# Kernel tuning notes

Hardware: AMD Instinct MI355X
Metric: run time of the kernel (lower is better)

## Reference

```python
import jax, jax.numpy as jnp
import numpy as np

B, T, F, H, S = 4096, 256, 64, 128, 32


def setup_inputs() -> dict:
    key = jax.random.key(0)
    ks = jax.random.split(key, 10)
    return {
        "x": jax.random.normal(ks[0], (B, T, F), jnp.float32),
        "static": jax.random.normal(ks[1], (B, S), jnp.float32),
        "hs0": jax.random.normal(ks[2], (B, H), jnp.float32),
        "cs0": jax.random.normal(ks[3], (B, H), jnp.float32),
        "W_ih": jax.random.normal(ks[4], (4 * H, F), jnp.float32) * 0.1,
        "W_hh": jax.random.normal(ks[5], (4 * H, H), jnp.float32) * 0.1,
        "b_ih": jax.random.normal(ks[6], (4 * H,), jnp.float32) * 0.1,
        "b_hh": jax.random.normal(ks[7], (4 * H,), jnp.float32) * 0.1,
        "W_lin": jax.random.normal(ks[8], (1, H + S), jnp.float32) * 0.1,
        "b_lin": jax.random.normal(ks[9], (1,), jnp.float32) * 0.1,
    }


def reference(x, static, hs0, cs0, W_ih, W_hh, b_ih, b_hh, W_lin, b_lin):
    # x: [B, T, F] -> time-major [T, B, F]; precompute input projections for all steps
    xs = jnp.swapaxes(x, 0, 1)
    px = jnp.einsum('tbf,gf->tbg', xs, W_ih) + b_ih  # [T, B, 4H]

    def step(carry, px_t):
        h, c = carry
        gates = px_t + h @ W_hh.T + b_hh  # [B, 4H]
        i, f, g, o = jnp.split(gates, 4, axis=-1)  # PyTorch LSTM gate order
        i = jax.nn.sigmoid(i)
        f = jax.nn.sigmoid(f)
        g = jnp.tanh(g)
        o = jax.nn.sigmoid(o)
        c = f * c + i * g
        h = o * jnp.tanh(c)
        return (h, c), None

    (h, c), _ = jax.lax.scan(step, (hs0, cs0), px)
    full = jnp.concatenate([h, static], axis=1)  # [B, H+S]
    return full @ W_lin.T + b_lin  # [B, 1]
```

## Files before the change

kernel.cpp:

```cpp
#include <hip/hip_runtime.h>
#include <hip/hip_bf16.h>

#define B_ 4096
#define T_ 256
#define F_ 64
#define H_ 128
#define S_ 32

typedef __attribute__((ext_vector_type(8))) short bf16x8;
typedef __attribute__((ext_vector_type(4))) float f32x4;

#define XS 72
#define HS 136

#define K1f (-1.4426950408889634f)
#define K2f (-2.8853900817779268f)

__device__ __forceinline__ float bf2f(unsigned short u) {
    unsigned v = (unsigned)u << 16;
    return __builtin_bit_cast(float, v);
}
__device__ __forceinline__ short f2bs(float f) {
    return (short)__bfloat16_as_ushort(__float2bfloat16(f));
}

#define LSTM_PHASE(XR, HR, HW, XW, STAGE_EN)                                      \
  {                                                                               \
    float2 xpre;                                                                  \
    const bool st_ = (STAGE_EN);                                                  \
    if (st_) xpre = *(const float2*)gxp;                                          \
    bf16x8 a[6];                                                                  \
    a[0] = *(const bf16x8*)&XR[fxb];                                              \
    a[1] = *(const bf16x8*)&XR[fxb + 32];                                         \
    a[2] = *(const bf16x8*)&HR[fhb];                                              \
    a[3] = *(const bf16x8*)&HR[fhb + 32];                                         \
    a[4] = *(const bf16x8*)&HR[fhb + 64];                                         \
    a[5] = *(const bf16x8*)&HR[fhb + 96];                                         \
    f32x4 ac[4];                                                                  \
    _Pragma("unroll")                                                             \
    for (int g = 0; g < 4; ++g)                                                   \
      ac[g] = __builtin_amdgcn_mfma_f32_16x16x32_bf16(wf[g][0], a[0], z4, 0, 0, 0); \
    _Pragma("unroll")                                                             \
    for (int kt = 1; kt < 6; ++kt) {                                              \
      _Pragma("unroll")                                                           \
      for (int g = 0; g < 4; ++g)                                                 \
        ac[g] = __builtin_amdgcn_mfma_f32_16x16x32_bf16(wf[g][kt], a[kt], ac[g], 0, 0, 0); \
    }                                                                             \
    float hn[4];                                                                  \
    _Pragma("unroll")                                                             \
    for (int q = 0; q < 4; ++q) {                                                 \
      const float ei = __builtin_amdgcn_exp2f(__builtin_fmaf(ac[0][q], K1f, bs0[q])); \
      const float i_ = __builtin_amdgcn_rcpf(1.0f + ei);                          \
      const float ef = __builtin_amdgcn_exp2f(__builtin_fmaf(ac[1][q], K1f, bs1[q])); \
      const float f_ = __builtin_amdgcn_rcpf(1.0f + ef);                          \
      const float eg = __builtin_amdgcn_exp2f(__builtin_fmaf(ac[2][q], K2f, btn[q])); \
      const float g_ = __builtin_fmaf(2.0f, __builtin_amdgcn_rcpf(1.0f + eg), -1.0f); \
      const float eo = __builtin_amdgcn_exp2f(__builtin_fmaf(ac[3][q], K1f, bs3[q])); \
      const float o_ = __builtin_amdgcn_rcpf(1.0f + eo);                          \
      const float cn = __builtin_fmaf(f_, c[q], i_ * g_);                         \
      c[q] = cn;                                                                  \
      const float ec = __builtin_amdgcn_exp2f(cn * K2f);                          \
      const float th = __builtin_fmaf(2.0f, __builtin_amdgcn_rcpf(1.0f + ec), -1.0f); \
      hn[q] = o_ * th;                                                            \
    }                                                                             \
    {                                                                             \
      float2 p0; p0.x = hn[0]; p0.y = hn[1];                                      \
      float2 p1; p1.x = hn[2]; p1.y = hn[3];                                      \
      __hip_bfloat162 b01 = __float22bfloat162_rn(p0);                            \
      __hip_bfloat162 b23 = __float22bfloat162_rn(p1);                            \
      uint2 uv; uv.x = *(unsigned*)&b01; uv.y = *(unsigned*)&b23;                 \
      *(uint2*)&HW[hwo] = uv;                                                     \
    }                                                                             \
    if (st_) {                                                                    \
      __hip_bfloat162 qx = __float22bfloat162_rn(xpre);                           \
      *(__hip_bfloat162*)&XW[xwo] = qx;                                           \
      gxp += F_;                                                                  \
    }                                                                             \
    __syncthreads();                                                              \
  }

__global__ __launch_bounds__(512, 2) void lstm_fused_kernel(
    const float* __restrict__ x,
    const float* __restrict__ statik,
    const float* __restrict__ hs0,
    const float* __restrict__ cs0,
    const float* __restrict__ W_ih,
    const float* __restrict__ W_hh,
    const float* __restrict__ b_ih,
    const float* __restrict__ b_hh,
    const float* __restrict__ W_lin,
    const float* __restrict__ b_lin,
    float* __restrict__ out)
{
    __shared__ unsigned short x_l[2][16 * XS];
    __shared__ unsigned short h_l[2][16 * HS];

    const int tid  = threadIdx.x;
    const int lane = tid & 63;
    const int w    = tid >> 6;
    const int b0   = blockIdx.x * 16;

    const int lrow = lane & 15;
    const int lkb  = lane >> 4;
    const int n0q  = w * 16 + lkb * 4;

    bf16x8 wf[4][6];
    #pragma unroll
    for (int g = 0; g < 4; ++g) {
        const int n = g * 128 + w * 16 + lrow;
        #pragma unroll
        for (int kt = 0; kt < 6; ++kt) {
            const int k0 = kt * 32 + lkb * 8;
            const float* src = (kt < 2) ? (W_ih + n * F_ + k0)
                                        : (W_hh + n * H_ + (k0 - 64));
            const float4 s0 = *(const float4*)(src);
            const float4 s1 = *(const float4*)(src + 4);
            bf16x8 v;
            v[0] = f2bs(s0.x); v[1] = f2bs(s0.y); v[2] = f2bs(s0.z); v[3] = f2bs(s0.w);
            v[4] = f2bs(s1.x); v[5] = f2bs(s1.y); v[6] = f2bs(s1.z); v[7] = f2bs(s1.w);
            wf[g][kt] = v;
        }
    }

    float bs0[4], bs1[4], btn[4], bs3[4];
    #pragma unroll
    for (int g = 0; g < 4; ++g) {
        const float4 bi = *(const float4*)(b_ih + g * 128 + n0q);
        const float4 bh = *(const float4*)(b_hh + g * 128 + n0q);
        const float bq[4] = {bi.x + bh.x, bi.y + bh.y, bi.z + bh.z, bi.w + bh.w};
        #pragma unroll
        for (int q = 0; q < 4; ++q) {
            if (g == 0)      bs0[q] = bq[q] * K1f;
            else if (g == 1) bs1[q] = bq[q] * K1f;
            else if (g == 2) btn[q] = bq[q] * K2f;
            else             bs3[q] = bq[q] * K1f;
        }
    }

    float c[4];
    {
        const float4 cv = *(const float4*)(cs0 + (size_t)(b0 + lrow) * H_ + n0q);
        c[0] = cv.x; c[1] = cv.y; c[2] = cv.z; c[3] = cv.w;
    }

    const int srow = tid >> 5;
    const int scp  = tid & 31;
    {
        const float* hp = hs0 + (size_t)(b0 + srow) * H_ + scp * 2;
        const float2 hv0 = *(const float2*)(hp);
        const float2 hv1 = *(const float2*)(hp + 64);
        __hip_bfloat162 q0 = __float22bfloat162_rn(hv0);
        __hip_bfloat162 q1 = __float22bfloat162_rn(hv1);
        *(__hip_bfloat162*)&h_l[0][srow * HS + scp * 2]      = q0;
        *(__hip_bfloat162*)&h_l[0][srow * HS + 64 + scp * 2] = q1;
    }
    const float* gxp = x + (size_t)(b0 + srow) * (T_ * F_) + scp * 2;
    {
        const float2 xv = *(const float2*)gxp;
        __hip_bfloat162 qx = __float22bfloat162_rn(xv);
        *(__hip_bfloat162*)&x_l[0][srow * XS + scp * 2] = qx;
    }
    gxp += F_;
    __syncthreads();

    const int fxb = lrow * XS + lkb * 8;
    const int fhb = lrow * HS + lkb * 8;
    const int hwo = lrow * HS + n0q;
    const int xwo = srow * XS + scp * 2;
    const f32x4 z4 = {0.0f, 0.0f, 0.0f, 0.0f};

    for (int t = 0; t < T_; t += 2) {
        LSTM_PHASE(x_l[0], h_l[0], h_l[1], x_l[1], true);
        LSTM_PHASE(x_l[1], h_l[1], h_l[0], x_l[0], (t + 2 < T_));
    }

    {
        const unsigned short* hf = h_l[0];
        const float wl0 = W_lin[lane];
        const float wl1 = W_lin[64 + lane];
        const float wl2 = (lane < S_) ? W_lin[128 + lane] : 0.0f;
        const float bl  = b_lin[0];
        #pragma unroll
        for (int rr = 0; rr < 2; ++rr) {
            const int r = w * 2 + rr;
            float p = bf2f(hf[r * HS + lane]) * wl0
                    + bf2f(hf[r * HS + 64 + lane]) * wl1;
            if (lane < S_) p += statik[(size_t)(b0 + r) * S_ + lane] * wl2;
            #pragma unroll
            for (int m = 32; m > 0; m >>= 1) p += __shfl_xor(p, m, 64);
            if (lane == 0) out[b0 + r] = p + bl;
        }
    }
}

extern "C" void kernel_launch(void* const* d_in, const int* in_sizes, int n_in,
                              void* d_out, int out_size, void* d_ws, size_t ws_size,
                              hipStream_t stream) {
    const float* x     = (const float*)d_in[0];
    const float* st    = (const float*)d_in[1];
    const float* hs0   = (const float*)d_in[2];
    const float* cs0   = (const float*)d_in[3];
    const float* W_ih  = (const float*)d_in[4];
    const float* W_hh  = (const float*)d_in[5];
    const float* b_ih  = (const float*)d_in[6];
    const float* b_hh  = (const float*)d_in[7];
    const float* W_lin = (const float*)d_in[8];
    const float* b_lin = (const float*)d_in[9];
    float* out = (float*)d_out;

    lstm_fused_kernel<<<dim3(B_ / 16), dim3(512), 0, stream>>>(
        x, st, hs0, cs0, W_ih, W_hh, b_ih, b_hh, W_lin, b_lin, out);
}
```

Baseline: 254.7 us.

## Load x directly into per-lane MFMA fragments, drop LDS staging of x

Each lane now loads its own x fragment for the input-projection MFMAs straight from global memory into registers, prefetching two steps ahead, and converts it to bf16 in registers. This removes the x shared-memory buffer, the staging stores and the LDS reads of x on every step. The barrier is replaced by an explicit lgkmcnt wait plus s_barrier, so it no longer waits on outstanding global loads. The cost is more VGPRs for the two in-flight x register sets and redundant global loads, since each x row is now read by several waves instead of once per block.

Result: slower. 316.0 us (+24.1%).

```diff
diff --git a/kernel.cpp b/kernel.cpp
--- a/kernel.cpp
+++ b/kernel.cpp
@@ -10,7 +10,6 @@
 typedef __attribute__((ext_vector_type(8))) short bf16x8;
 typedef __attribute__((ext_vector_type(4))) float f32x4;
 
-#define XS 72
 #define HS 136
 
 #define K1f (-1.4426950408889634f)
@@ -24,38 +23,67 @@
     return (short)__bfloat16_as_ushort(__float2bfloat16(f));
 }
 
-#define LSTM_PHASE(XR, HR, HW, XW, STAGE_EN)                                      \
+struct XReg { float4 a, b, c, d; };
+
+#define PHASE(XR, HR, HW, TL)                                                     \
   {                                                                               \
-    float2 xpre;                                                                  \
-    const bool st_ = (STAGE_EN);                                                  \
-    if (st_) xpre = *(const float2*)gxp;                                          \
-    bf16x8 a[6];                                                                  \
-    a[0] = *(const bf16x8*)&XR[fxb];                                              \
-    a[1] = *(const bf16x8*)&XR[fxb + 32];                                         \
-    a[2] = *(const bf16x8*)&HR[fhb];                                              \
-    a[3] = *(const bf16x8*)&HR[fhb + 32];                                         \
-    a[4] = *(const bf16x8*)&HR[fhb + 64];                                         \
-    a[5] = *(const bf16x8*)&HR[fhb + 96];                                         \
-    f32x4 ac[4];                                                                  \
-    _Pragma("unroll")                                                             \
-    for (int g = 0; g < 4; ++g)                                                   \
-      ac[g] = __builtin_amdgcn_mfma_f32_16x16x32_bf16(wf[g][0], a[0], z4, 0, 0, 0); \
-    _Pragma("unroll")                                                             \
-    for (int kt = 1; kt < 6; ++kt) {                                              \
-      _Pragma("unroll")                                                           \
-      for (int g = 0; g < 4; ++g)                                                 \
-        ac[g] = __builtin_amdgcn_mfma_f32_16x16x32_bf16(wf[g][kt], a[kt], ac[g], 0, 0, 0); \
-    }                                                                             \
+                        \
+    bf16x8 a0 = *(const bf16x8*)&HR[fhb];                                         \
+    bf16x8 a1 = *(const bf16x8*)&HR[fhb + 32];                                    \
+    bf16x8 a2 = *(const bf16x8*)&HR[fhb + 64];                                    \
+    bf16x8 a3 = *(const bf16x8*)&HR[fhb + 96];                                    \
+          \
+    bf16x8 fx0, fx1;                                                              \
+    fx0[0] = f2bs(XR.a.x); fx0[1] = f2bs(XR.a.y); fx0[2] = f2bs(XR.a.z);          \
+    fx0[3] = f2bs(XR.a.w); fx0[4] = f2bs(XR.b.x); fx0[5] = f2bs(XR.b.y);          \
+    fx0[6] = f2bs(XR.b.z); fx0[7] = f2bs(XR.b.w);                                 \
+    fx1[0] = f2bs(XR.c.x); fx1[1] = f2bs(XR.c.y); fx1[2] = f2bs(XR.c.z);          \
+    fx1[3] = f2bs(XR.c.w); fx1[4] = f2bs(XR.d.x); fx1[5] = f2bs(XR.d.y);          \
+    fx1[6] = f2bs(XR.d.z); fx1[7] = f2bs(XR.d.w);                                 \
+         \
+    { const float* lp_ = gxl + (size_t)(TL) * F_;                                 \
+      XR.a = *(const float4*)(lp_);                                               \
+      XR.b = *(const float4*)(lp_ + 4);                                           \
+      XR.c = *(const float4*)(lp_ + 32);                                          \
+      XR.d = *(const float4*)(lp_ + 36); }                                        \
+            \
+    f32x4 ac0, ac1, ac2, ac3;                                                     \
+    ac0 = __builtin_amdgcn_mfma_f32_16x16x32_bf16(wf[0][0], fx0, z4, 0, 0, 0);    \
+    ac1 = __builtin_amdgcn_mfma_f32_16x16x32_bf16(wf[1][0], fx0, z4, 0, 0, 0);    \
+    ac2 = __builtin_amdgcn_mfma_f32_16x16x32_bf16(wf[2][0], fx0, z4, 0, 0, 0);    \
+    ac3 = __builtin_amdgcn_mfma_f32_16x16x32_bf16(wf[3][0], fx0, z4, 0, 0, 0);    \
+    ac0 = __builtin_amdgcn_mfma_f32_16x16x32_bf16(wf[0][1], fx1, ac0, 0, 0, 0);   \
+    ac1 = __builtin_amdgcn_mfma_f32_16x16x32_bf16(wf[1][1], fx1, ac1, 0, 0, 0);   \
+    ac2 = __builtin_amdgcn_mfma_f32_16x16x32_bf16(wf[2][1], fx1, ac2, 0, 0, 0);   \
+    ac3 = __builtin_amdgcn_mfma_f32_16x16x32_bf16(wf[3][1], fx1, ac3, 0, 0, 0);   \
+                                                                      \
+    ac0 = __builtin_amdgcn_mfma_f32_16x16x32_bf16(wf[0][2], a0, ac0, 0, 0, 0);    \
+    ac1 = __builtin_amdgcn_mfma_f32_16x16x32_bf16(wf[1][2], a0, ac1, 0, 0, 0);    \
+    ac2 = __builtin_amdgcn_mfma_f32_16x16x32_bf16(wf[2][2], a0, ac2, 0, 0, 0);    \
+    ac3 = __builtin_amdgcn_mfma_f32_16x16x32_bf16(wf[3][2], a0, ac3, 0, 0, 0);    \
+    ac0 = __builtin_amdgcn_mfma_f32_16x16x32_bf16(wf[0][3], a1, ac0, 0, 0, 0);    \
+    ac1 = __builtin_amdgcn_mfma_f32_16x16x32_bf16(wf[1][3], a1, ac1, 0, 0, 0);    \
+    ac2 = __builtin_amdgcn_mfma_f32_16x16x32_bf16(wf[2][3], a1, ac2, 0, 0, 0);    \
+    ac3 = __builtin_amdgcn_mfma_f32_16x16x32_bf16(wf[3][3], a1, ac3, 0, 0, 0);    \
+    ac0 = __builtin_amdgcn_mfma_f32_16x16x32_bf16(wf[0][4], a2, ac0, 0, 0, 0);    \
+    ac1 = __builtin_amdgcn_mfma_f32_16x16x32_bf16(wf[1][4], a2, ac1, 0, 0, 0);    \
+    ac2 = __builtin_amdgcn_mfma_f32_16x16x32_bf16(wf[2][4], a2, ac2, 0, 0, 0);    \
+    ac3 = __builtin_amdgcn_mfma_f32_16x16x32_bf16(wf[3][4], a2, ac3, 0, 0, 0);    \
+    ac0 = __builtin_amdgcn_mfma_f32_16x16x32_bf16(wf[0][5], a3, ac0, 0, 0, 0);    \
+    ac1 = __builtin_amdgcn_mfma_f32_16x16x32_bf16(wf[1][5], a3, ac1, 0, 0, 0);    \
+    ac2 = __builtin_amdgcn_mfma_f32_16x16x32_bf16(wf[2][5], a3, ac2, 0, 0, 0);    \
+    ac3 = __builtin_amdgcn_mfma_f32_16x16x32_bf16(wf[3][5], a3, ac3, 0, 0, 0);    \
+                                                  \
     float hn[4];                                                                  \
     _Pragma("unroll")                                                             \
     for (int q = 0; q < 4; ++q) {                                                 \
-      const float ei = __builtin_amdgcn_exp2f(__builtin_fmaf(ac[0][q], K1f, bs0[q])); \
+      const float ei = __builtin_amdgcn_exp2f(__builtin_fmaf(ac0[q], K1f, bs0[q])); \
       const float i_ = __builtin_amdgcn_rcpf(1.0f + ei);                          \
-      const float ef = __builtin_amdgcn_exp2f(__builtin_fmaf(ac[1][q], K1f, bs1[q])); \
+      const float ef = __builtin_amdgcn_exp2f(__builtin_fmaf(ac1[q], K1f, bs1[q])); \
       const float f_ = __builtin_amdgcn_rcpf(1.0f + ef);                          \
-      const float eg = __builtin_amdgcn_exp2f(__builtin_fmaf(ac[2][q], K2f, btn[q])); \
+      const float eg = __builtin_amdgcn_exp2f(__builtin_fmaf(ac2[q], K2f, btn[q])); \
       const float g_ = __builtin_fmaf(2.0f, __builtin_amdgcn_rcpf(1.0f + eg), -1.0f); \
-      const float eo = __builtin_amdgcn_exp2f(__builtin_fmaf(ac[3][q], K1f, bs3[q])); \
+      const float eo = __builtin_amdgcn_exp2f(__builtin_fmaf(ac3[q], K1f, bs3[q])); \
       const float o_ = __builtin_amdgcn_rcpf(1.0f + eo);                          \
       const float cn = __builtin_fmaf(f_, c[q], i_ * g_);                         \
       c[q] = cn;                                                                  \
@@ -63,20 +91,14 @@
       const float th = __builtin_fmaf(2.0f, __builtin_amdgcn_rcpf(1.0f + ec), -1.0f); \
       hn[q] = o_ * th;                                                            \
     }                                                                             \
-    {                                                                             \
-      float2 p0; p0.x = hn[0]; p0.y = hn[1];                                      \
-      float2 p1; p1.x = hn[2]; p1.y = hn[3];                                      \
-      __hip_bfloat162 b01 = __float22bfloat162_rn(p0);                            \
-      __hip_bfloat162 b23 = __float22bfloat162_rn(p1);                            \
-      uint2 uv; uv.x = *(unsigned*)&b01; uv.y = *(unsigned*)&b23;                 \
-      *(uint2*)&HW[hwo] = uv;                                                     \
-    }                                                                             \
-    if (st_) {                                                                    \
-      __hip_bfloat162 qx = __float22bfloat162_rn(xpre);                           \
-      *(__hip_bfloat162*)&XW[xwo] = qx;                                           \
-      gxp += F_;                                                                  \
-    }                                                                             \
-    __syncthreads();                                                              \
+    { unsigned lo = (unsigned)(unsigned short)f2bs(hn[0])                         \
+                  | ((unsigned)(unsigned short)f2bs(hn[1]) << 16);                \
+      unsigned hi = (unsigned)(unsigned short)f2bs(hn[2])                         \
+                  | ((unsigned)(unsigned short)f2bs(hn[3]) << 16);                \
+      uint2 uv; uv.x = lo; uv.y = hi;                                             \
+      *(uint2*)&HW[hwo] = uv; }                                                   \
+    asm volatile("s_waitcnt lgkmcnt(0)" ::: "memory");                            \
+    __builtin_amdgcn_s_barrier();                                                 \
   }
 
 __global__ __launch_bounds__(512, 2) void lstm_fused_kernel(
@@ -92,7 +114,6 @@
     const float* __restrict__ b_lin,
     float* __restrict__ out)
 {
-    __shared__ unsigned short x_l[2][16 * XS];
     __shared__ unsigned short h_l[2][16 * HS];
 
     const int tid  = threadIdx.x;
@@ -143,35 +164,41 @@
         c[0] = cv.x; c[1] = cv.y; c[2] = cv.z; c[3] = cv.w;
     }
 
-    const int srow = tid >> 5;
-    const int scp  = tid & 31;
+    const float* gxl = x + (size_t)(b0 + lrow) * (T_ * F_) + lkb * 8;
+
     {
+        const int srow = tid >> 5;
+        const int scp  = tid & 31;
         const float* hp = hs0 + (size_t)(b0 + srow) * H_ + scp * 2;
         const float2 hv0 = *(const float2*)(hp);
         const float2 hv1 = *(const float2*)(hp + 64);
-        __hip_bfloat162 q0 = __float22bfloat162_rn(hv0);
-        __hip_bfloat162 q1 = __float22bfloat162_rn(hv1);
-        *(__hip_bfloat162*)&h_l[0][srow * HS + scp * 2]      = q0;
-        *(__hip_bfloat162*)&h_l[0][srow * HS + 64 + scp * 2] = q1;
-    }
-    const float* gxp = x + (size_t)(b0 + srow) * (T_ * F_) + scp * 2;
-    {
-        const float2 xv = *(const float2*)gxp;
-        __hip_bfloat162 qx = __float22bfloat162_rn(xv);
-        *(__hip_bfloat162*)&x_l[0][srow * XS + scp * 2] = qx;
-    }
-    gxp += F_;
+        unsigned q0 = (unsigned)(unsigned short)f2bs(hv0.x)
+                    | ((unsigned)(unsigned short)f2bs(hv0.y) << 16);
+        unsigned q1 = (unsigned)(unsigned short)f2bs(hv1.x)
+                    | ((unsigned)(unsigned short)f2bs(hv1.y) << 16);
+        *(unsigned*)&h_l[0][srow * HS + scp * 2]      = q0;
+        *(unsigned*)&h_l[0][srow * HS + 64 + scp * 2] = q1;
+    }
+    XReg xr0, xr1;
+    xr0.a = *(const float4*)(gxl);
+    xr0.b = *(const float4*)(gxl + 4);
+    xr0.c = *(const float4*)(gxl + 32);
+    xr0.d = *(const float4*)(gxl + 36);
+    xr1.a = *(const float4*)(gxl + F_);
+    xr1.b = *(const float4*)(gxl + F_ + 4);
+    xr1.c = *(const float4*)(gxl + F_ + 32);
+    xr1.d = *(const float4*)(gxl + F_ + 36);
     __syncthreads();
 
-    const int fxb = lrow * XS + lkb * 8;
     const int fhb = lrow * HS + lkb * 8;
     const int hwo = lrow * HS + n0q;
-    const int xwo = srow * XS + scp * 2;
     const f32x4 z4 = {0.0f, 0.0f, 0.0f, 0.0f};
 
     for (int t = 0; t < T_; t += 2) {
-        LSTM_PHASE(x_l[0], h_l[0], h_l[1], x_l[1], true);
-        LSTM_PHASE(x_l[1], h_l[1], h_l[0], x_l[0], (t + 2 < T_));
+        const int tl0 = (t + 2 < T_) ? t + 2 : T_ - 1;
+        const int tl1 = (t + 3 < T_) ? t + 3 : T_ - 1;
+        PHASE(xr0, h_l[0], h_l[1], tl0);
+        PHASE(xr1, h_l[1], h_l[0], tl1);
     }
 
     {
```

## Precompute next step's input-projection MFMAs off the critical path and swizzle LDS

Applied to the files above, without the earlier changes.

Splits the per-step MFMA chain so the x·W_ih part for the next timestep is issued after the gate math and carried in registers, leaving only the 4 h-dependent k-tiles on the recurrent critical path. The x staging becomes a 4-deep ring with a register-held prefetch several steps ahead. Padded LDS rows are replaced by XOR-swizzled layouts to avoid bank conflicts. The __syncthreads is replaced by an explicit lgkmcnt wait plus s_barrier. This adds register pressure and makes the buffer-index logic more delicate.

New measurement: 228.6 us. 10.2% less time.

```diff
diff --git a/kernel.cpp b/kernel.cpp
--- a/kernel.cpp
+++ b/kernel.cpp
@@ -10,11 +10,10 @@
 typedef __attribute__((ext_vector_type(8))) short bf16x8;
 typedef __attribute__((ext_vector_type(4))) float f32x4;
 
-#define XS 72
-#define HS 136
-
 #define K1f (-1.4426950408889634f)
 #define K2f (-2.8853900817779268f)
+
+#define MF(A, B, C) __builtin_amdgcn_mfma_f32_16x16x32_bf16((A), (B), (C), 0, 0, 0)
 
 __device__ __forceinline__ float bf2f(unsigned short u) {
     unsigned v = (unsigned)u << 16;
@@ -24,59 +23,61 @@
     return (short)__bfloat16_as_ushort(__float2bfloat16(f));
 }
 
-#define LSTM_PHASE(XR, HR, HW, XW, STAGE_EN)                                      \
-  {                                                                               \
-    float2 xpre;                                                                  \
-    const bool st_ = (STAGE_EN);                                                  \
-    if (st_) xpre = *(const float2*)gxp;                                          \
-    bf16x8 a[6];                                                                  \
-    a[0] = *(const bf16x8*)&XR[fxb];                                              \
-    a[1] = *(const bf16x8*)&XR[fxb + 32];                                         \
-    a[2] = *(const bf16x8*)&HR[fhb];                                              \
-    a[3] = *(const bf16x8*)&HR[fhb + 32];                                         \
-    a[4] = *(const bf16x8*)&HR[fhb + 64];                                         \
-    a[5] = *(const bf16x8*)&HR[fhb + 96];                                         \
-    f32x4 ac[4];                                                                  \
-    _Pragma("unroll")                                                             \
-    for (int g = 0; g < 4; ++g)                                                   \
-      ac[g] = __builtin_amdgcn_mfma_f32_16x16x32_bf16(wf[g][0], a[0], z4, 0, 0, 0); \
-    _Pragma("unroll")                                                             \
-    for (int kt = 1; kt < 6; ++kt) {                                              \
-      _Pragma("unroll")                                                           \
-      for (int g = 0; g < 4; ++g)                                                 \
-        ac[g] = __builtin_amdgcn_mfma_f32_16x16x32_bf16(wf[g][kt], a[kt], ac[g], 0, 0, 0); \
-    }                                                                             \
-    float hn[4];                                                                  \
-    _Pragma("unroll")                                                             \
-    for (int q = 0; q < 4; ++q) {                                                 \
-      const float ei = __builtin_amdgcn_exp2f(__builtin_fmaf(ac[0][q], K1f, bs0[q])); \
-      const float i_ = __builtin_amdgcn_rcpf(1.0f + ei);                          \
-      const float ef = __builtin_amdgcn_exp2f(__builtin_fmaf(ac[1][q], K1f, bs1[q])); \
-      const float f_ = __builtin_amdgcn_rcpf(1.0f + ef);                          \
-      const float eg = __builtin_amdgcn_exp2f(__builtin_fmaf(ac[2][q], K2f, btn[q])); \
+#define PHASE(HR, HW, XW, XN, TLD)                                               \
+  {                                                                              \
+    const char* hr_ = (const char*)(HR);                                         \
+    bf16x8 a0 = *(const bf16x8*)(hr_ + fh0);                                     \
+    bf16x8 a1 = *(const bf16x8*)(hr_ + fh1);                                     \
+    bf16x8 a2 = *(const bf16x8*)(hr_ + fh2);                                     \
+    bf16x8 a3 = *(const bf16x8*)(hr_ + fh3);                                     \
+                    \
+    { __hip_bfloat162 qx = __float22bfloat162_rn(xheld);                         \
+      *(__hip_bfloat162*)((char*)(XW) + xws) = qx; }                             \
+    xheld = *(const float2*)(gxs + (size_t)(TLD) * F_);                          \
+                                          \
+    f32x4 ac0 = sd0, ac1 = sd1, ac2 = sd2, ac3 = sd3;                            \
+    ac0 = MF(wf[0][2], a0, ac0); ac1 = MF(wf[1][2], a0, ac1);                    \
+    ac2 = MF(wf[2][2], a0, ac2); ac3 = MF(wf[3][2], a0, ac3);                    \
+    ac0 = MF(wf[0][3], a1, ac0); ac1 = MF(wf[1][3], a1, ac1);                    \
+    ac2 = MF(wf[2][3], a1, ac2); ac3 = MF(wf[3][3], a1, ac3);                    \
+    ac0 = MF(wf[0][4], a2, ac0); ac1 = MF(wf[1][4], a2, ac1);                    \
+    ac2 = MF(wf[2][4], a2, ac2); ac3 = MF(wf[3][4], a2, ac3);                    \
+    ac0 = MF(wf[0][5], a3, ac0); ac1 = MF(wf[1][5], a3, ac1);                    \
+    ac2 = MF(wf[2][5], a3, ac2); ac3 = MF(wf[3][5], a3, ac3);                    \
+                                                 \
+    float hn[4];                                                                 \
+    _Pragma("unroll")                                                            \
+    for (int q = 0; q < 4; ++q) {                                                \
+      const float ei = __builtin_amdgcn_exp2f(__builtin_fmaf(ac0[q], K1f, bs0[q])); \
+      const float i_ = __builtin_amdgcn_rcpf(1.0f + ei);                         \
+      const float ef = __builtin_amdgcn_exp2f(__builtin_fmaf(ac1[q], K1f, bs1[q])); \
+      const float f_ = __builtin_amdgcn_rcpf(1.0f + ef);                         \
+      const float eg = __builtin_amdgcn_exp2f(__builtin_fmaf(ac2[q], K2f, btn[q])); \
       const float g_ = __builtin_fmaf(2.0f, __builtin_amdgcn_rcpf(1.0f + eg), -1.0f); \
-      const float eo = __builtin_amdgcn_exp2f(__builtin_fmaf(ac[3][q], K1f, bs3[q])); \
-      const float o_ = __builtin_amdgcn_rcpf(1.0f + eo);                          \
-      const float cn = __builtin_fmaf(f_, c[q], i_ * g_);                         \
-      c[q] = cn;                                                                  \
-      const float ec = __builtin_amdgcn_exp2f(cn * K2f);                          \
+      const float eo = __builtin_amdgcn_exp2f(__builtin_fmaf(ac3[q], K1f, bs3[q])); \
+      const float o_ = __builtin_amdgcn_rcpf(1.0f + eo);                         \
+      const float cn = __builtin_fmaf(f_, c[q], i_ * g_);                        \
+      c[q] = cn;                                                                 \
+      const float ec = __builtin_amdgcn_exp2f(cn * K2f);                         \
       const float th = __builtin_fmaf(2.0f, __builtin_amdgcn_rcpf(1.0f + ec), -1.0f); \
-      hn[q] = o_ * th;                                                            \
-    }                                                                             \
-    {                                                                             \
-      float2 p0; p0.x = hn[0]; p0.y = hn[1];                                      \
-      float2 p1; p1.x = hn[2]; p1.y = hn[3];                                      \
-      __hip_bfloat162 b01 = __float22bfloat162_rn(p0);                            \
-      __hip_bfloat162 b23 = __float22bfloat162_rn(p1);                            \
-      uint2 uv; uv.x = *(unsigned*)&b01; uv.y = *(unsigned*)&b23;                 \
-      *(uint2*)&HW[hwo] = uv;                                                     \
-    }                                                                             \
-    if (st_) {                                                                    \
-      __hip_bfloat162 qx = __float22bfloat162_rn(xpre);                           \
-      *(__hip_bfloat162*)&XW[xwo] = qx;                                           \
-      gxp += F_;                                                                  \
-    }                                                                             \
-    __syncthreads();                                                              \
+      hn[q] = o_ * th;                                                           \
+    }                                                                            \
+    { float2 p0; p0.x = hn[0]; p0.y = hn[1];                                     \
+      float2 p1; p1.x = hn[2]; p1.y = hn[3];                                     \
+      __hip_bfloat162 b01 = __float22bfloat162_rn(p0);                           \
+      __hip_bfloat162 b23 = __float22bfloat162_rn(p1);                           \
+      uint2 uv; uv.x = *(unsigned*)&b01; uv.y = *(unsigned*)&b23;                \
+      *(uint2*)((char*)(HW) + hwb) = uv; }                                       \
+              \
+    { const char* xn_ = (const char*)(XN);                                       \
+      bf16x8 nf0 = *(const bf16x8*)(xn_ + fx0);                                  \
+      bf16x8 nf1 = *(const bf16x8*)(xn_ + fx1);                                  \
+      sd0 = MF(wf[0][0], nf0, z4); sd1 = MF(wf[1][0], nf0, z4);                  \
+      sd2 = MF(wf[2][0], nf0, z4); sd3 = MF(wf[3][0], nf0, z4);                  \
+      sd0 = MF(wf[0][1], nf1, sd0); sd1 = MF(wf[1][1], nf1, sd1);                \
+      sd2 = MF(wf[2][1], nf1, sd2); sd3 = MF(wf[3][1], nf1, sd3); }              \
+    asm volatile("s_waitcnt lgkmcnt(0)" ::: "memory");                           \
+    __builtin_amdgcn_s_barrier();                                                \
   }
 
 __global__ __launch_bounds__(512, 2) void lstm_fused_kernel(
@@ -92,8 +93,8 @@
     const float* __restrict__ b_lin,
     float* __restrict__ out)
 {
-    __shared__ unsigned short x_l[2][16 * XS];
-    __shared__ unsigned short h_l[2][16 * HS];
+    __shared__ __align__(16) unsigned short h_l[2][16 * 128];
+    __shared__ __align__(16) unsigned short x_l[4][16 * 64];
 
     const int tid  = threadIdx.x;
     const int lane = tid & 63;
@@ -143,48 +144,80 @@
         c[0] = cv.x; c[1] = cv.y; c[2] = cv.z; c[3] = cv.w;
     }
 
+    const int fsw = (lrow & 7) << 4;
+    const int fx0 = lrow * 128 + ((lkb * 16) ^ fsw);
+    const int fx1 = lrow * 128 + ((64 + lkb * 16) ^ fsw);
+    const int fh0 = lrow * 256 + ((0   + lkb * 16) ^ fsw);
+    const int fh1 = lrow * 256 + ((64  + lkb * 16) ^ fsw);
+    const int fh2 = lrow * 256 + ((128 + lkb * 16) ^ fsw);
+    const int fh3 = lrow * 256 + ((192 + lkb * 16) ^ fsw);
+    const int hwb = lrow * 256 + ((n0q * 2) ^ fsw);
+
     const int srow = tid >> 5;
     const int scp  = tid & 31;
+    const int ssw  = (srow & 7) << 4;
+    const int xws  = srow * 128 + ((scp * 4) ^ ssw);
+
+    const float* gxs = x + (size_t)(b0 + srow) * (T_ * F_) + scp * 2;
+    float2 xheld;
     {
         const float* hp = hs0 + (size_t)(b0 + srow) * H_ + scp * 2;
         const float2 hv0 = *(const float2*)(hp);
         const float2 hv1 = *(const float2*)(hp + 64);
         __hip_bfloat162 q0 = __float22bfloat162_rn(hv0);
         __hip_bfloat162 q1 = __float22bfloat162_rn(hv1);
-        *(__hip_bfloat162*)&h_l[0][srow * HS + scp * 2]      = q0;
-        *(__hip_bfloat162*)&h_l[0][srow * HS + 64 + scp * 2] = q1;
-    }
-    const float* gxp = x + (size_t)(b0 + srow) * (T_ * F_) + scp * 2;
-    {
-        const float2 xv = *(const float2*)gxp;
-        __hip_bfloat162 qx = __float22bfloat162_rn(xv);
-        *(__hip_bfloat162*)&x_l[0][srow * XS + scp * 2] = qx;
-    }
-    gxp += F_;
+        *(__hip_bfloat162*)((char*)h_l[0] + srow * 256 + ((scp * 4) ^ ssw))       = q0;
+        *(__hip_bfloat162*)((char*)h_l[0] + srow * 256 + ((128 + scp * 4) ^ ssw)) = q1;
+
+        const float2 x0 = *(const float2*)(gxs);
+        const float2 x1 = *(const float2*)(gxs + F_);
+        __hip_bfloat162 qa = __float22bfloat162_rn(x0);
+        __hip_bfloat162 qb = __float22bfloat162_rn(x1);
+        *(__hip_bfloat162*)((char*)x_l[0] + xws) = qa;
+        *(__hip_bfloat162*)((char*)x_l[1] + xws) = qb;
+        xheld = *(const float2*)(gxs + 2 * F_);
+    }
     __syncthreads();
 
-    const int fxb = lrow * XS + lkb * 8;
-    const int fhb = lrow * HS + lkb * 8;
-    const int hwo = lrow * HS + n0q;
-    const int xwo = srow * XS + scp * 2;
     const f32x4 z4 = {0.0f, 0.0f, 0.0f, 0.0f};
 
-    for (int t = 0; t < T_; t += 2) {
-        LSTM_PHASE(x_l[0], h_l[0], h_l[1], x_l[1], true);
-        LSTM_PHASE(x_l[1], h_l[1], h_l[0], x_l[0], (t + 2 < T_));
-    }
-
-    {
-        const unsigned short* hf = h_l[0];
+    f32x4 sd0, sd1, sd2, sd3;
+    {
+        const char* xn_ = (const char*)x_l[0];
+        bf16x8 nf0 = *(const bf16x8*)(xn_ + fx0);
+        bf16x8 nf1 = *(const bf16x8*)(xn_ + fx1);
+        sd0 = MF(wf[0][0], nf0, z4); sd1 = MF(wf[1][0], nf0, z4);
+        sd2 = MF(wf[2][0], nf0, z4); sd3 = MF(wf[3][0], nf0, z4);
+        sd0 = MF(wf[0][1], nf1, sd0); sd1 = MF(wf[1][1], nf1, sd1);
+        sd2 = MF(wf[2][1], nf1, sd2); sd3 = MF(wf[3][1], nf1, sd3);
+    }
+
+    for (int t = 0; t < T_; t += 4) {
+        const int t3 = (t + 3 < T_) ? t + 3 : T_ - 1;
+        const int t4 = (t + 4 < T_) ? t + 4 : T_ - 1;
+        const int t5 = (t + 5 < T_) ? t + 5 : T_ - 1;
+        const int t6 = (t + 6 < T_) ? t + 6 : T_ - 1;
+        PHASE(h_l[0], h_l[1], x_l[2], x_l[1], t3);
+        PHASE(h_l[1], h_l[0], x_l[3], x_l[2], t4);
+        PHASE(h_l[0], h_l[1], x_l[0], x_l[3], t5);
+        PHASE(h_l[1], h_l[0], x_l[1], x_l[0], t6);
+    }
+
+    {
+        const char* hf = (const char*)h_l[0];
         const float wl0 = W_lin[lane];
         const float wl1 = W_lin[64 + lane];
         const float wl2 = (lane < S_) ? W_lin[128 + lane] : 0.0f;
         const float bl  = b_lin[0];
         #pragma unroll
         for (int rr = 0; rr < 2; ++rr) {
-            const int r = w * 2 + rr;
-            float p = bf2f(hf[r * HS + lane]) * wl0
-                    + bf2f(hf[r * HS + 64 + lane]) * wl1;
+            const int r  = w * 2 + rr;
+            const int rs = (r & 7) << 4;
+            const unsigned short h0 =
+                *(const unsigned short*)(hf + r * 256 + ((2 * lane) ^ rs));
+            const unsigned short h1 =
+                *(const unsigned short*)(hf + r * 256 + ((128 + 2 * lane) ^ rs));
+            float p = bf2f(h0) * wl0 + bf2f(h1) * wl1;
             if (lane < S_) p += statik[(size_t)(b0 + r) * S_ + lane] * wl2;
             #pragma unroll
             for (int m = 32; m > 0; m >>= 1) p += __shfl_xor(p, m, 64);
```
